# Kernel optimization log

Hardware: AMD Instinct MI355X
Metric: run time of the kernel (lower is better)

The kernel has to match this reference:

```python
import jax, jax.numpy as jnp
import numpy as np

SQRT_2_OVER_PI = 0.7978845608028654  # sqrt(2/pi)

def gelu_tanh(x):
    # F.gelu(x, approximate='tanh')
    return 0.5 * x * (1.0 + jnp.tanh(SQRT_2_OVER_PI * (x + 0.044715 * x * x * x)))

def setup_inputs() -> dict:
    key = jax.random.key(0)
    k1, k2, k3, k4 = jax.random.split(key, 4)
    B, S, DIN, DOUT = 8, 2048, 1152, 4608
    hidden_states = jax.random.normal(k1, (B, S, DIN), dtype=jnp.float32)
    # simulated int8 quantized weights (symmetric, per-output-channel scale)
    w_int8 = jax.random.randint(k2, (DOUT, DIN), -127, 128, dtype=jnp.int32)
    w_scale = jax.random.uniform(k3, (DOUT,), dtype=jnp.float32, minval=0.001, maxval=0.01)
    bias = jax.random.normal(k4, (DOUT,), dtype=jnp.float32) * 0.02
    return {"hidden_states": hidden_states, "w_int8": w_int8, "w_scale": w_scale, "bias": bias}

def reference(hidden_states, w_int8, w_scale, bias):
    # dequantize: per-output-channel scale
    w = w_int8.astype(hidden_states.dtype) * w_scale[:, None]  # [DOUT, DIN]
    # linear projection: [B,S,DIN] @ [DIN,DOUT] -> [B,S,DOUT]
    proj = jnp.einsum('bsd,od->bso', hidden_states, w) + bias
    return gelu_tanh(proj)
```

## Files before the change

### kernel.cpp

```cpp
#include <hip/hip_runtime.h>
#include <cstdint>
#include <cstddef>

#define M_DIM 16384
#define N_DIM 4608
#define K_DIM 1152
#define NKT   (K_DIM / 128)

typedef __attribute__((ext_vector_type(8))) __bf16 bf16x8;
typedef __attribute__((ext_vector_type(4))) float  f32x4;
typedef __attribute__((ext_vector_type(4))) int    v4i;

__device__ __forceinline__ unsigned short f2bf(float f) {
    unsigned int u = __float_as_uint(f);
    unsigned int r = (u + 0x7FFFu + ((u >> 16) & 1u)) >> 16;
    return (unsigned short)r;
}

__device__ __forceinline__ float gelu_tanh_f(float v) {
    float u = 0.7978845608028654f * (v + 0.044715f * v * v * v);
    float a = fabsf(u);
    float t = __expf(-2.0f * a);
    float th = (1.0f - t) / (1.0f + t);
    th = (u < 0.0f) ? -th : th;
    return 0.5f * v * (1.0f + th);
}

#define QA_BLOCKS (M_DIM / 4)
#define W4_COUNT  ((N_DIM * K_DIM) / 4)
#define PW_BLOCKS ((W4_COUNT + 255) / 256)

__global__ void prepass(const float* __restrict__ A,
                        const int* __restrict__ w,
                        signed char* __restrict__ qa,
                        float* __restrict__ sA,
                        signed char* __restrict__ qw) {
    if (blockIdx.x < QA_BLOCKS) {
        const int lane = threadIdx.x & 63;
        const int row  = blockIdx.x * 4 + (threadIdx.x >> 6);
        const float2* src = (const float2*)(A + (size_t)row * K_DIM);
        float2 v[9];
        float amax = 0.f;
#pragma unroll
        for (int j = 0; j < 9; ++j) {
            v[j] = src[j * 64 + lane];
            amax = fmaxf(amax, fmaxf(fabsf(v[j].x), fabsf(v[j].y)));
        }
#pragma unroll
        for (int off = 32; off > 0; off >>= 1)
            amax = fmaxf(amax, __shfl_xor(amax, off));
        amax = fmaxf(amax, 1e-30f);
        float inv = 127.0f / amax;
        if (lane == 0) sA[row] = amax * (1.0f / 127.0f);
        char2* dst = (char2*)(qa + (size_t)row * K_DIM);
#pragma unroll
        for (int j = 0; j < 9; ++j) {
            char2 o;
            o.x = (signed char)__float2int_rn(v[j].x * inv);
            o.y = (signed char)__float2int_rn(v[j].y * inv);
            dst[j * 64 + lane] = o;
        }
    } else {
        int i = (blockIdx.x - QA_BLOCKS) * 256 + threadIdx.x;
        if (i >= W4_COUNT) return;
        int4 v = ((const int4*)w)[i];
        char4 o;
        o.x = (signed char)v.x; o.y = (signed char)v.y;
        o.z = (signed char)v.z; o.w = (signed char)v.w;
        ((char4*)qw)[i] = o;
    }
}


template <int MH, int NH>
__device__ __forceinline__ void mfma_quad(v4i (&acc)[2][4][2][2],
                                          v4i (&a)[4][2],
                                          v4i (&b)[2][2][2]) {
    __builtin_amdgcn_s_setprio(1);
#pragma unroll
    for (int s = 0; s < 2; ++s)
#pragma unroll
        for (int mt = 0; mt < 4; ++mt)
#pragma unroll
            for (int nt = 0; nt < 2; ++nt)
                acc[MH][mt][NH][nt] = __builtin_amdgcn_mfma_i32_16x16x64_i8(
                    a[mt][s], b[NH][nt][s], acc[MH][mt][NH][nt], 0, 0, 0);
    __builtin_amdgcn_s_setprio(0);
}

__global__ __launch_bounds__(512, 2) void qgemm_i8_8phase(
    const signed char* __restrict__ Aq,
    const signed char* __restrict__ Wq,
    const float* __restrict__ sA,
    const float* __restrict__ w_scale,
    const float* __restrict__ bias,
    float* __restrict__ out) {
    __shared__ __align__(16) signed char lds[2][2][256 * 128];

    const int tid    = threadIdx.x;
    const int l      = tid & 63;
    const int wv     = tid >> 6;
    const int lane16 = l & 15;
    const int quad   = l >> 4;

    const int bid = blockIdx.x;
    const int swz = (bid & 7) * (1152 / 8) + (bid >> 3);
    const int mt0 = (swz / 18) * 256;
    const int nt0 = (swz % 18) * 256;

    const int wm = (wv & 1) * 128;
    const int wn = (wv >> 1) * 64;

    auto stage_half = [&](int buf, int mat, int half, int kt) {
        const signed char* gbase =
            (mat == 0) ? (Aq + (size_t)mt0 * K_DIM) : (Wq + (size_t)nt0 * K_DIM);
#pragma unroll
        for (int j = 0; j < 2; ++j) {
            int q   = j * 512 + tid;
            int row = half * 128 + (q >> 3);
            int c   = (q & 7) ^ (row & 7);
            const signed char* g = gbase + (size_t)row * K_DIM + kt * 128 + c * 16;
            signed char* d = &lds[buf][mat][half * 16384 + (j * 512 + wv * 64) * 16];
            __builtin_amdgcn_global_load_lds(
                (const __attribute__((address_space(1))) unsigned int*)g,
                (__attribute__((address_space(3))) unsigned int*)d, 16, 0, 0);
        }
    };

    v4i acc[2][4][2][2];
#pragma unroll
    for (int mh = 0; mh < 2; ++mh)
#pragma unroll
        for (int mt = 0; mt < 4; ++mt)
#pragma unroll
            for (int nh = 0; nh < 2; ++nh)
#pragma unroll
                for (int nt = 0; nt < 2; ++nt)
                    acc[mh][mt][nh][nt] = v4i{0, 0, 0, 0};

    v4i a[4][2];
    v4i b[2][2][2];

    auto ldA = [&](int cur, int mh, int mt, int s) -> v4i {
        int r = wm + mh * 64 + mt * 16 + lane16;
        int p = (s * 4 + quad) ^ (r & 7);
        return *(const v4i*)&lds[cur][0][r * 128 + p * 16];
    };
    auto ldB = [&](int cur, int nh, int nt, int s) -> v4i {
        int r = wn + nh * 32 + nt * 16 + lane16;
        int p = (s * 4 + quad) ^ (r & 7);
        return *(const v4i*)&lds[cur][1][r * 128 + p * 16];
    };

    stage_half(0, 0, 0, 0); stage_half(0, 0, 1, 0);
    stage_half(0, 1, 0, 0); stage_half(0, 1, 1, 0);
    stage_half(1, 1, 0, 1); stage_half(1, 1, 1, 1);
    asm volatile("s_waitcnt vmcnt(4)" ::: "memory");
    __builtin_amdgcn_sched_barrier(0);
    __builtin_amdgcn_s_barrier();

    for (int kt = 0; kt < NKT; ++kt) {
        const int cur = kt & 1, nxt = cur ^ 1;
#pragma unroll
        for (int mt = 0; mt < 4; ++mt)
#pragma unroll
            for (int s = 0; s < 2; ++s) a[mt][s] = ldA(cur, 0, mt, s);
#pragma unroll
        for (int nt = 0; nt < 2; ++nt)
#pragma unroll
            for (int s = 0; s < 2; ++s) b[0][nt][s] = ldB(cur, 0, nt, s);
        if (kt + 1 < NKT) stage_half(nxt, 0, 0, kt + 1);
        __builtin_amdgcn_s_barrier();
        mfma_quad<0, 0>(acc, a, b);
        __builtin_amdgcn_s_barrier();
#pragma unroll
        for (int nt = 0; nt < 2; ++nt)
#pragma unroll
            for (int s = 0; s < 2; ++s) b[1][nt][s] = ldB(cur, 1, nt, s);
        if (kt + 1 < NKT) stage_half(nxt, 0, 1, kt + 1);
        __builtin_amdgcn_s_barrier();
        mfma_quad<0, 1>(acc, a, b);
        __builtin_amdgcn_s_barrier();
#pragma unroll
        for (int mt = 0; mt < 4; ++mt)
#pragma unroll
            for (int s = 0; s < 2; ++s) a[mt][s] = ldA(cur, 1, mt, s);
        if (kt + 2 < NKT) stage_half(cur, 1, 0, kt + 2);
        __builtin_amdgcn_s_barrier();
        mfma_quad<1, 1>(acc, a, b);
        __builtin_amdgcn_s_barrier();
        if (kt + 2 < NKT) stage_half(cur, 1, 1, kt + 2);
        mfma_quad<1, 0>(acc, a, b);
        if (kt + 2 < NKT) {
            asm volatile("s_waitcnt vmcnt(4)" ::: "memory");
        } else if (kt + 1 < NKT) {
            asm volatile("s_waitcnt vmcnt(0)" ::: "memory");
        }
        __builtin_amdgcn_sched_barrier(0);
        __builtin_amdgcn_s_barrier();
    }

#pragma unroll
    for (int nh = 0; nh < 2; ++nh)
#pragma unroll
        for (int nt = 0; nt < 2; ++nt) {
            int n    = nt0 + wn + nh * 32 + nt * 16 + lane16;
            float sc = w_scale[n];
            float bi = bias[n];
#pragma unroll
            for (int mh = 0; mh < 2; ++mh)
#pragma unroll
                for (int mt = 0; mt < 4; ++mt) {
                    int mbase = mt0 + wm + mh * 64 + mt * 16 + quad * 4;
#pragma unroll
                    for (int r = 0; r < 4; ++r) {
                        float v = (float)acc[mh][mt][nh][nt][r] * sA[mbase + r] * sc + bi;
                        __builtin_nontemporal_store(
                            gelu_tanh_f(v), &out[(size_t)(mbase + r) * N_DIM + n]);
                    }
                }
        }
}

__global__ void qgelu_gemm_bf16_fused(const float* __restrict__ Af,
                                      const int* __restrict__ Wi,
                                      const float* __restrict__ w_scale,
                                      const float* __restrict__ bias,
                                      float* __restrict__ out) {
    __shared__ __align__(16) unsigned short As[128 * 64];
    __shared__ __align__(16) unsigned short Bs[128 * 64];

    const int tid    = threadIdx.x;
    const int l      = tid & 63;
    const int wv     = tid >> 6;
    const int lane16 = l & 15;
    const int quad   = l >> 4;
    const int m0 = blockIdx.x * 128;
    const int n0 = blockIdx.y * 128;
    const int wm = (wv & 1) * 64;
    const int wn = (wv >> 1) * 64;

    f32x4 acc[4][4];
#pragma unroll
    for (int i = 0; i < 4; ++i)
#pragma unroll
        for (int j = 0; j < 4; ++j) acc[i][j] = f32x4{0.f, 0.f, 0.f, 0.f};

    for (int kt = 0; kt < K_DIM / 64; ++kt) {
        __syncthreads();
#pragma unroll
        for (int i = 0; i < 8; ++i) {
            int g    = i * 256 + tid;
            int row  = g >> 4;
            int grp  = g & 15;
            int c    = grp >> 1;
            int half = g & 1;
            int p    = c ^ (row & 7);
            int off  = row * 64 + p * 8 + half * 4;
            {
                float4 v = *(const float4*)(Af + (size_t)(m0 + row) * K_DIM + kt * 64 + grp * 4);
                ushort4 o;
                o.x = f2bf(v.x); o.y = f2bf(v.y); o.z = f2bf(v.z); o.w = f2bf(v.w);
                *(ushort4*)(As + off) = o;
            }
            {
                int4 v = *(const int4*)(Wi + (size_t)(n0 + row) * K_DIM + kt * 64 + grp * 4);
                ushort4 o;
                o.x = f2bf((float)v.x); o.y = f2bf((float)v.y);
                o.z = f2bf((float)v.z); o.w = f2bf((float)v.w);
                *(ushort4*)(Bs + off) = o;
            }
        }
        __syncthreads();

#pragma unroll
        for (int s = 0; s < 2; ++s) {
            bf16x8 af[4], bfr[4];
#pragma unroll
            for (int mt = 0; mt < 4; ++mt) {
                int row = wm + mt * 16 + lane16;
                int p   = (s * 4 + quad) ^ (row & 7);
                af[mt]  = *(const bf16x8*)(As + row * 64 + p * 8);
            }
#pragma unroll
            for (int nt = 0; nt < 4; ++nt) {
                int row = wn + nt * 16 + lane16;
                int p   = (s * 4 + quad) ^ (row & 7);
                bfr[nt] = *(const bf16x8*)(Bs + row * 64 + p * 8);
            }
#pragma unroll
            for (int mt = 0; mt < 4; ++mt)
#pragma unroll
                for (int nt = 0; nt < 4; ++nt)
                    acc[mt][nt] = __builtin_amdgcn_mfma_f32_16x16x32_bf16(
                        af[mt], bfr[nt], acc[mt][nt], 0, 0, 0);
        }
    }

#pragma unroll
    for (int nt = 0; nt < 4; ++nt) {
        int n    = n0 + wn + nt * 16 + lane16;
        float sc = w_scale[n];
        float bi = bias[n];
#pragma unroll
        for (int mt = 0; mt < 4; ++mt) {
#pragma unroll
            for (int r = 0; r < 4; ++r) {
                int m   = m0 + wm + mt * 16 + quad * 4 + r;
                float v = acc[mt][nt][r] * sc + bi;
                __builtin_nontemporal_store(
                    gelu_tanh_f(v), &out[(size_t)m * N_DIM + n]);
            }
        }
    }
}

extern "C" void kernel_launch(void* const* d_in, const int* in_sizes, int n_in,
                              void* d_out, int out_size, void* d_ws, size_t ws_size,
                              hipStream_t stream) {
    const float* hs   = (const float*)d_in[0];
    const int*   w8   = (const int*)d_in[1];
    const float* wsc  = (const float*)d_in[2];
    const float* bias = (const float*)d_in[3];
    float* out = (float*)d_out;

    const size_t nA = (size_t)M_DIM * K_DIM;
    const size_t nW = (size_t)N_DIM * K_DIM;
    const size_t need = nA + nW + (size_t)M_DIM * sizeof(float);

    if (ws_size >= need) {
        signed char* qa = (signed char*)d_ws;
        signed char* qw = qa + nA;
        float* sA = (float*)(qa + nA + nW);
        prepass<<<QA_BLOCKS + PW_BLOCKS, 256, 0, stream>>>(hs, w8, qa, sA, qw);
        qgemm_i8_8phase<<<dim3((M_DIM / 256) * (N_DIM / 256)), 512, 0, stream>>>(
            qa, qw, sA, wsc, bias, out);
    } else {
        dim3 grid(M_DIM / 128, N_DIM / 128);
        qgelu_gemm_bf16_fused<<<grid, 256, 0, stream>>>(hs, w8, wsc, bias, out);
    }
}
```

Measured before the change: 460.4 us.

## Stage GEMM epilogue through swizzled LDS for 16-byte coalesced output stores

The epilogue now writes GELU results into a per-wave XOR-swizzled LDS scratch area and reads them back as float4 rows, so each lane stores 16 contiguous bytes instead of scattered 4-byte stores. It also hoists the scale and bias loads and loads the row scales as vectors. GELU is rewritten as the algebraically equivalent v*sigmoid(2u) form with a single exp and divide. The cost is extra LDS traffic, waitcnt stalls, and reuse of the pipeline LDS buffer after a barrier.

New measurement: 444.1 us. 1.04x faster.

```diff
diff --git a/kernel.cpp b/kernel.cpp
--- a/kernel.cpp
+++ b/kernel.cpp
@@ -18,12 +18,10 @@
 }
 
 __device__ __forceinline__ float gelu_tanh_f(float v) {
-    float u = 0.7978845608028654f * (v + 0.044715f * v * v * v);
-    float a = fabsf(u);
-    float t = __expf(-2.0f * a);
-    float th = (1.0f - t) / (1.0f + t);
-    th = (u < 0.0f) ? -th : th;
-    return 0.5f * v * (1.0f + th);
+    float v2 = v * v;
+    float u2 = v * fmaf(v2, 0.07135481627260093f, 1.5957691216057308f);
+    float e  = __expf(-u2);
+    return v / (1.0f + e);
 }
 
 #define QA_BLOCKS (M_DIM / 4)
@@ -200,25 +198,54 @@
         __builtin_amdgcn_s_barrier();
     }
 
+    __syncthreads();
+
+    float sc[2][2], bi[2][2];
 #pragma unroll
     for (int nh = 0; nh < 2; ++nh)
 #pragma unroll
         for (int nt = 0; nt < 2; ++nt) {
-            int n    = nt0 + wn + nh * 32 + nt * 16 + lane16;
-            float sc = w_scale[n];
-            float bi = bias[n];
-#pragma unroll
-            for (int mh = 0; mh < 2; ++mh)
-#pragma unroll
-                for (int mt = 0; mt < 4; ++mt) {
-                    int mbase = mt0 + wm + mh * 64 + mt * 16 + quad * 4;
+            int n = nt0 + wn + nh * 32 + nt * 16 + lane16;
+            sc[nh][nt] = w_scale[n];
+            bi[nh][nt] = bias[n];
+        }
+
+    float* scr = (float*)(&lds[1][0][0]) + wv * 1024;
+    const int lo3 = lane16 & 3;
+
+#pragma unroll
+    for (int mh = 0; mh < 2; ++mh)
+#pragma unroll
+        for (int mt = 0; mt < 4; ++mt) {
+            const int rbase = mt0 + wm + mh * 64 + mt * 16;
+            const f32x4 sa = *(const f32x4*)(sA + rbase + quad * 4);
+#pragma unroll
+            for (int nh = 0; nh < 2; ++nh)
+#pragma unroll
+                for (int nt = 0; nt < 2; ++nt) {
+                    const int col   = nh * 32 + nt * 16 + lane16;
+                    const int chunk = col >> 2;
 #pragma unroll
                     for (int r = 0; r < 4; ++r) {
-                        float v = (float)acc[mh][mt][nh][nt][r] * sA[mbase + r] * sc + bi;
-                        __builtin_nontemporal_store(
-                            gelu_tanh_f(v), &out[(size_t)(mbase + r) * N_DIM + n]);
+                        const int row16 = quad * 4 + r;
+                        const int c2    = chunk ^ row16;
+                        float v = (float)acc[mh][mt][nh][nt][r] * sa[r] * sc[nh][nt] + bi[nh][nt];
+                        scr[row16 * 64 + c2 * 4 + lo3] = gelu_tanh_f(v);
                     }
                 }
+            asm volatile("s_waitcnt lgkmcnt(0)" ::: "memory");
+            __builtin_amdgcn_sched_barrier(0);
+#pragma unroll
+            for (int s = 0; s < 4; ++s) {
+                const int row16 = s * 4 + quad;
+                const int c2    = lane16 ^ row16;
+                f32x4 val = *(const f32x4*)(scr + row16 * 64 + c2 * 4);
+                __builtin_nontemporal_store(
+                    val, (f32x4*)(out + (size_t)(rbase + row16) * N_DIM
+                                  + nt0 + wn + lane16 * 4));
+            }
+            asm volatile("s_waitcnt lgkmcnt(0)" ::: "memory");
+            __builtin_amdgcn_sched_barrier(0);
         }
 }
 
```
